# Kernel tuning notes

Hardware: AMD Instinct MI355X
Metric: run time of the kernel (lower is better)

## Reference

```python
import jax, jax.numpy as jnp
import numpy as np

N, E = 10000, 320000
C = 64          # channel multiplicity of 0e and 1o node features
A = 4           # node_attrs (species one-hot) dim
NB = 8          # radial basis size (edge_embedding dim)
H = 8           # invariant_neurons
AVG_NEIGH = 32.0
LOG2 = 0.6931471805599453

def ssp(x):
    # ShiftedSoftPlus
    return jax.nn.softplus(x) - LOG2


def setup_inputs() -> dict:
    key = jax.random.key(0)
    ks = jax.random.split(key, 13)
    d = dict(
        node_features=jax.random.normal(ks[0], (N, 4 * C), jnp.float32),   # [N, C + 3C]
        node_attrs=jax.random.normal(ks[1], (N, A), jnp.float32),
        edge_attrs=jax.random.normal(ks[2], (E, 4), jnp.float32),          # sh l=0,1
        edge_embedding=jax.random.uniform(ks[3], (E, NB), jnp.float32),
        edge_index=jax.random.randint(ks[4], (2, E), 0, N),
        # e3nn Linear (internal weights) per-l blocks
        W_lin1_0=jax.random.normal(ks[5], (C, C), jnp.float32),
        W_lin1_1=jax.random.normal(ks[6], (C, C), jnp.float32),
        # radial FullyConnectedNet: NB -> H -> 4C (tp.weight_numel)
        W_fc1=jax.random.normal(ks[7], (NB, H), jnp.float32),
        W_fc2=jax.random.normal(ks[8], (H, 4 * C), jnp.float32),
        # linear_2: irreps_mid.simplify() = 2Cx0e+2Cx1o -> Cx0e+Cx1o
        W_lin2_0=jax.random.normal(ks[9], (2 * C, C), jnp.float32),
        W_lin2_1=jax.random.normal(ks[10], (2 * C, C), jnp.float32),
        # self-connection FullyConnectedTensorProduct weights (node_attrs are scalars)
        W_sc0=jax.random.normal(ks[11], (C, A, C), jnp.float32),
        W_sc1=jax.random.normal(ks[12], (C, A, C), jnp.float32),
    )
    return d


def _forward(node_features, node_attrs, edge_attrs, edge_embedding, edge_index,
             W_lin1_0, W_lin1_1, W_fc1, W_fc2, W_lin2_0, W_lin2_1, W_sc0, W_sc1):
    n = node_features.shape[0]
    e = edge_attrs.shape[0]
    x0 = node_features[:, :C]                      # [N, C]   scalars (0e)
    x1 = node_features[:, C:].reshape(n, C, 3)     # [N, C, 3] vectors (1o)

    # self-connection: FullyConnectedTensorProduct(feat, node_attrs(0e)) -> feat
    sc_norm = 1.0 / np.sqrt(C * A)
    sc0 = jnp.einsum('nu,na,uav->nv', x0, node_attrs, W_sc0) * sc_norm
    sc1 = jnp.einsum('num,na,uav->nvm', x1, node_attrs, W_sc1) * sc_norm

    # linear_1 (per-irrep mixing, e3nn normalization 1/sqrt(fan_in))
    y0 = (x0 @ W_lin1_0) / np.sqrt(C)
    y1 = jnp.einsum('num,uv->nvm', x1, W_lin1_1) / np.sqrt(C)

    # radial MLP -> per-edge TP weights [E, 4C] (instruction order p1..p4)
    h = ssp((edge_embedding @ W_fc1) / np.sqrt(NB))
    w = (h @ W_fc2) / np.sqrt(H)
    wp1, wp2, wp3, wp4 = jnp.split(w, 4, axis=1)   # each [E, C]

    src = edge_index[1]
    dst = edge_index[0]
    xs0 = y0[src]                                  # [E, C]
    xs1 = y1[src]                                  # [E, C, 3]
    sh0 = edge_attrs[:, :1]                        # [E, 1]
    sh1 = edge_attrs[:, 1:4]                       # [E, 3]

    # uvu tensor product paths (component normalization)
    mid_s0 = wp1 * xs0 * sh0                                            # 0e x 0e -> 0e
    mid_s1 = wp4 * jnp.einsum('eum,em->eu', xs1, sh1) / np.sqrt(3.0)    # 1o x 1o -> 0e
    mid_v0 = (wp2 * xs0)[:, :, None] * sh1[:, None, :]                  # 0e x 1o -> 1o
    mid_v1 = wp3[:, :, None] * xs1 * sh0[:, :, None]                    # 1o x 0e -> 1o

    edge_feat = jnp.concatenate(
        [mid_s0, mid_s1, mid_v0.reshape(e, 3 * C), mid_v1.reshape(e, 3 * C)], axis=1
    )                                                                    # [E, 8C]

    # scatter-sum to destination nodes, then divide by sqrt(avg_num_neighbors)
    agg = jnp.zeros((n, 8 * C), edge_feat.dtype).at[dst].add(edge_feat)
    agg = agg / np.sqrt(AVG_NEIGH)

    s = agg[:, :2 * C]                              # [N, 2C] scalars
    v = agg[:, 2 * C:].reshape(n, 2 * C, 3)         # [N, 2C, 3] vectors

    # linear_2 on simplified mid irreps
    o0 = (s @ W_lin2_0) / np.sqrt(2 * C) + sc0
    o1 = jnp.einsum('num,uv->nvm', v, W_lin2_1) / np.sqrt(2 * C) + sc1

    return jnp.concatenate([o0, o1.reshape(n, 3 * C)], axis=1)          # [N, 4C]


def reference(node_features, node_attrs, edge_attrs, edge_embedding, edge_index,
              W_lin1_0, W_lin1_1, W_fc1, W_fc2, W_lin2_0, W_lin2_1, W_sc0, W_sc1):
    return _forward(node_features, node_attrs, edge_attrs, edge_embedding, edge_index,
                    W_lin1_0, W_lin1_1, W_fc1, W_fc2, W_lin2_0, W_lin2_1, W_sc0, W_sc1)
```

## Files before the change

### kernel.cpp

```cpp
#include <hip/hip_runtime.h>


__device__ __forceinline__ unsigned short f2b(float f) {
  unsigned u = __float_as_uint(f);
  return (unsigned short)((u + 0x7FFFu + ((u >> 16) & 1u)) >> 16);
}
__device__ __forceinline__ unsigned packb(float a, float b) {
  return (unsigned)f2b(a) | ((unsigned)f2b(b) << 16);
}
__device__ __forceinline__ float blo(unsigned p) { return __uint_as_float(p << 16); }
__device__ __forceinline__ float bhi(unsigned p) { return __uint_as_float(p & 0xFFFF0000u); }
__device__ __forceinline__ float b2f(unsigned short h) {
  return __uint_as_float((unsigned)h << 16);
}

__global__ __launch_bounds__(256) void k_pack(
    const float* __restrict__ W10, const float* __restrict__ W11,
    const float* __restrict__ Ws0, const float* __restrict__ Ws1,
    const float* __restrict__ W20, const float* __restrict__ W21,
    unsigned* __restrict__ wpk1, unsigned* __restrict__ wpks,
    unsigned* __restrict__ wpk2a, unsigned* __restrict__ wpk2b) {
  int i = blockIdx.x * 256 + threadIdx.x;
  if (i < 4096) wpk1[i] = packb(W10[i], W11[i]);
  else if (i < 4096 + 16384) {
    int j = i - 4096;
    wpks[j] = packb(Ws0[j], Ws1[j]);
  } else if (i < 4096 + 16384 + 4096) {
    int j = i - (4096 + 16384);
    wpk2a[j] = packb(W20[j], W20[4096 + j]);
  } else if (i < 4096 + 16384 + 8192) {
    int j = i - (4096 + 16384 + 4096);
    wpk2b[j] = packb(W21[j], W21[4096 + j]);
  }
}

__global__ __launch_bounds__(256) void k_hist(const int* __restrict__ ei,
                                              int* __restrict__ cnt, int nedges) {
  int e = blockIdx.x * 256 + threadIdx.x;
  if (e < nedges) atomicAdd(&cnt[ei[e]], 1);
}

__global__ __launch_bounds__(1024) void k_scan(const int* __restrict__ cnt,
                                               int* __restrict__ offs,
                                               int* __restrict__ cur,
                                               int nnodes, int nedges) {
  __shared__ int s_wtot[16], s_wpre[16];
  const int tid = threadIdx.x;
  const int lane = tid & 63;
  const int w = tid >> 6;
  int vals[16];
  int tot = 0;
  const int start = tid * 16;
#pragma unroll
  for (int k = 0; k < 16; ++k) {
    int i = start + k;
    int c = (i < nnodes) ? cnt[i] : 0;
    vals[k] = c;
    tot += c;
  }
  int incl = tot;
#pragma unroll
  for (int off = 1; off < 64; off <<= 1) {
    int v = __shfl_up(incl, off, 64);
    if (lane >= off) incl += v;
  }
  if (lane == 63) s_wtot[w] = incl;
  __syncthreads();
  if (tid == 0) {
    int run = 0;
#pragma unroll
    for (int i = 0; i < 16; ++i) { s_wpre[i] = run; run += s_wtot[i]; }
  }
  __syncthreads();
  int run = s_wpre[w] + (incl - tot);
#pragma unroll
  for (int k = 0; k < 16; ++k) {
    int i = start + k;
    if (i < nnodes) {
      offs[i] = run;
      cur[i] = run;
      run += vals[k];
    }
  }
  if (tid == 0) offs[nnodes] = nedges;
}

__global__ __launch_bounds__(256) void k_build(
    const int* __restrict__ ei, const float* __restrict__ ee,
    const float* __restrict__ ea, const float* __restrict__ Wf1,
    int* __restrict__ cur, int* __restrict__ srcs,
    uint4* __restrict__ erec, int nedges) {
  __shared__ float s_w[64];
  const int tid = threadIdx.x;
  if (tid < 64) s_w[tid] = Wf1[tid];
  __syncthreads();
  int e = blockIdx.x * 256 + tid;
  if (e >= nedges) return;
  const int d = ei[e];
  const int s = ei[nedges + e];
  const int p = atomicAdd(&cur[d], 1);
  srcs[p] = s;
  const float4 a = *(const float4*)(ee + (size_t)e * 8);
  const float4 b = *(const float4*)(ee + (size_t)e * 8 + 4);
  float r[8];
  const float is8 = 0.35355339059327379f;
#pragma unroll
  for (int j = 0; j < 8; ++j) {
    float dd = a.x * s_w[0 * 8 + j] + a.y * s_w[1 * 8 + j] + a.z * s_w[2 * 8 + j] +
               a.w * s_w[3 * 8 + j] + b.x * s_w[4 * 8 + j] + b.y * s_w[5 * 8 + j] +
               b.z * s_w[6 * 8 + j] + b.w * s_w[7 * 8 + j];
    dd *= is8;
    float sp = fmaxf(dd, 0.f) + log1pf(__expf(-fabsf(dd)));
    r[j] = (sp - 0.69314718055994531f) * is8;
  }
  const float4 sh = *(const float4*)(ea + (size_t)e * 4);
  erec[(size_t)p * 2] = make_uint4(packb(r[0], r[1]), packb(r[2], r[3]),
                                   packb(r[4], r[5]), packb(r[6], r[7]));
  erec[(size_t)p * 2 + 1] =
      make_uint4(__float_as_uint(sh.x), __float_as_uint(sh.y),
                 __float_as_uint(sh.z), __float_as_uint(sh.w));
}

__global__ __launch_bounds__(256) void k_node_pre(
    const float* __restrict__ nf, const float* __restrict__ na,
    const unsigned* __restrict__ wpk1, const unsigned* __restrict__ wpks,
    unsigned short* __restrict__ yqb, float* __restrict__ out, int nnodes) {
  __shared__ unsigned s_w1[4096];
  __shared__ unsigned s_ws[16384];
  __shared__ float s_nf[16][256];
  __shared__ float s_na[16][4];
  const int tid = threadIdx.x;
  const int lane = tid & 63;
  const int wv = tid >> 6;

  for (int i = tid; i < 4096; i += 256) s_w1[i] = wpk1[i];
  for (int i = tid; i < 16384; i += 256) s_ws[i] = wpks[i];

  const int ngroups = (nnodes + 15) / 16;
  for (int g = blockIdx.x; g < ngroups; g += gridDim.x) {
    const int base = g * 16;
    __syncthreads();
    for (int i = tid; i < 16 * 256; i += 256) {
      int r = i >> 8, c = i & 255;
      int n = base + r;
      s_nf[r][c] = (n < nnodes) ? nf[(size_t)n * 256 + c] : 0.f;
    }
    if (tid < 64) {
      int r = tid >> 2, c = tid & 3;
      int n = base + r;
      s_na[r][c] = (n < nnodes) ? na[(size_t)n * 4 + c] : 0.f;
    }
    __syncthreads();

    const int r0 = wv * 4;
    const int v = lane;
    float y0a[4] = {0.f, 0.f, 0.f, 0.f};
    float y1a[4][3] = {};
    float sc0a[4] = {0.f, 0.f, 0.f, 0.f};
    float sc1a[4][3] = {};

#pragma unroll 4
    for (int u = 0; u < 64; ++u) {
      float x0r[4], x1r[4][3];
#pragma unroll
      for (int r = 0; r < 4; ++r) {
        x0r[r] = s_nf[r0 + r][u];
#pragma unroll
        for (int m = 0; m < 3; ++m) x1r[r][m] = s_nf[r0 + r][64 + u * 3 + m];
      }
      const unsigned q1 = s_w1[u * 64 + v];
      const float w0 = blo(q1);
      const float w1 = bhi(q1);
#pragma unroll
      for (int r = 0; r < 4; ++r) {
        y0a[r] = fmaf(x0r[r], w0, y0a[r]);
#pragma unroll
        for (int m = 0; m < 3; ++m) y1a[r][m] = fmaf(x1r[r][m], w1, y1a[r][m]);
      }
#pragma unroll
      for (int a = 0; a < 4; ++a) {
        const unsigned qs = s_ws[(u * 4 + a) * 64 + v];
        const float ws0 = blo(qs);
        const float ws1 = bhi(qs);
#pragma unroll
        for (int r = 0; r < 4; ++r) {
          const float nav = s_na[r0 + r][a];
          sc0a[r] = fmaf(x0r[r] * nav, ws0, sc0a[r]);
          const float t = nav * ws1;
#pragma unroll
          for (int m = 0; m < 3; ++m)
            sc1a[r][m] = fmaf(x1r[r][m], t, sc1a[r][m]);
        }
      }
    }

#pragma unroll
    for (int r = 0; r < 4; ++r) {
      const int n = base + r0 + r;
      if (n < nnodes) {
        ushort4 yv;
        yv.x = f2b(y0a[r] * 0.125f);
        yv.y = f2b(y1a[r][0] * 0.125f);
        yv.z = f2b(y1a[r][1] * 0.125f);
        yv.w = f2b(y1a[r][2] * 0.125f);
        *(ushort4*)(yqb + ((size_t)n * 64 + v) * 4) = yv;
        out[(size_t)n * 256 + v] = sc0a[r] * 0.0625f;
#pragma unroll
        for (int m = 0; m < 3; ++m)
          out[(size_t)n * 256 + 64 + v * 3 + m] = sc1a[r][m] * 0.0625f;
      }
    }
  }
}

__global__ __launch_bounds__(256, 4) void k_agg(
    const unsigned short* __restrict__ yqb, const uint4* __restrict__ erec,
    const int* __restrict__ srcs, const int* __restrict__ offs,
    const float* __restrict__ Wf2, unsigned short* __restrict__ aggb, int nnodes) {
  const int tid = threadIdx.x;
  const int u = tid & 63;
  const int wv = tid >> 6;
  const int n = blockIdx.x * 4 + wv;
  if (n >= nnodes) return;

  float wreg[32];
#pragma unroll
  for (int j = 0; j < 8; ++j)
#pragma unroll
    for (int q = 0; q < 4; ++q) wreg[j * 4 + q] = Wf2[j * 256 + q * 64 + u];

  float as0 = 0.f, as1 = 0.f;
  float av0[3] = {0.f, 0.f, 0.f};
  float av1[3] = {0.f, 0.f, 0.f};

  const int beg = offs[n], end = offs[n + 1];
#pragma unroll 4
  for (int i = beg; i < end; ++i) {
    const int src = srcs[i];
    const ushort4 yb = *(const ushort4*)(yqb + ((size_t)src * 64 + u) * 4);
    const uint4 hp = erec[(size_t)i * 2];
    const uint4 shu = erec[(size_t)i * 2 + 1];
    const float4 sh = make_float4(__uint_as_float(shu.x), __uint_as_float(shu.y),
                                  __uint_as_float(shu.z), __uint_as_float(shu.w));
    const float hv[8] = {blo(hp.x), bhi(hp.x), blo(hp.y), bhi(hp.y),
                         blo(hp.z), bhi(hp.z), blo(hp.w), bhi(hp.w)};
    float wp[4] = {0.f, 0.f, 0.f, 0.f};
#pragma unroll
    for (int j = 0; j < 8; ++j)
#pragma unroll
      for (int q = 0; q < 4; ++q) wp[q] = fmaf(hv[j], wreg[j * 4 + q], wp[q]);
    const float y0 = b2f(yb.x), y1 = b2f(yb.y), y2 = b2f(yb.z), y3 = b2f(yb.w);
    const float dot3 = y1 * sh.y + y2 * sh.z + y3 * sh.w;
    as0 = fmaf(wp[0] * y0, sh.x, as0);
    as1 = fmaf(wp[3], dot3, as1);
    const float t2 = wp[1] * y0;
    av0[0] = fmaf(t2, sh.y, av0[0]);
    av0[1] = fmaf(t2, sh.z, av0[1]);
    av0[2] = fmaf(t2, sh.w, av0[2]);
    const float t3 = wp[2] * sh.x;
    av1[0] = fmaf(t3, y1, av1[0]);
    av1[1] = fmaf(t3, y2, av1[1]);
    av1[2] = fmaf(t3, y3, av1[2]);
  }

  unsigned short* ap = aggb + (size_t)n * 512;
  ap[u] = f2b(as0);
  ap[64 + u] = f2b(as1 * 0.57735026918962576f);
#pragma unroll
  for (int m = 0; m < 3; ++m) {
    ap[128 + m * 64 + u] = f2b(av0[m]);
    ap[320 + m * 64 + u] = f2b(av1[m]);
  }
}

__global__ __launch_bounds__(256, 4) void k_lin2(
    const unsigned short* __restrict__ aggb, const unsigned* __restrict__ wpk2a,
    const unsigned* __restrict__ wpk2b, float* __restrict__ out, int nnodes) {
  __shared__ float s_x[4][4][512];
  const int tid = threadIdx.x;
  const int u = tid & 63;
  const int wv = tid >> 6;
  const int nb = blockIdx.x * 16 + wv * 4;

#pragma unroll
  for (int r = 0; r < 4; ++r) {
    const int n = nb + r;
    if (n < nnodes) {
      const uint4 aw = *(const uint4*)(aggb + (size_t)n * 512 + u * 8);
      float4* dst = (float4*)&s_x[wv][r][u * 8];
      dst[0] = make_float4(blo(aw.x), bhi(aw.x), blo(aw.y), bhi(aw.y));
      dst[1] = make_float4(blo(aw.z), bhi(aw.z), blo(aw.w), bhi(aw.w));
    }
  }

  float o0[4] = {0.f, 0.f, 0.f, 0.f};
  float o1[4][3] = {};

#pragma unroll 2
  for (int up = 0; up < 64; ++up) {
    const unsigned qa = wpk2a[up * 64 + u];
    const unsigned qb = wpk2b[up * 64 + u];
    const float w20a = blo(qa), w20b = bhi(qa);
    const float w21a = blo(qb), w21b = bhi(qb);
#pragma unroll
    for (int r = 0; r < 4; ++r) {
      o0[r] = fmaf(s_x[wv][r][up], w20a, o0[r]);
      o0[r] = fmaf(s_x[wv][r][64 + up], w20b, o0[r]);
#pragma unroll
      for (int m = 0; m < 3; ++m) {
        o1[r][m] = fmaf(s_x[wv][r][128 + m * 64 + up], w21a, o1[r][m]);
        o1[r][m] = fmaf(s_x[wv][r][320 + m * 64 + up], w21b, o1[r][m]);
      }
    }
  }

  const float scl = 1.f / 64.f;
#pragma unroll
  for (int r = 0; r < 4; ++r) {
    const int n = nb + r;
    if (n < nnodes) {
      out[(size_t)n * 256 + u] += o0[r] * scl;
#pragma unroll
      for (int m = 0; m < 3; ++m)
        out[(size_t)n * 256 + 64 + u * 3 + m] += o1[r][m] * scl;
    }
  }
}

extern "C" void kernel_launch(void* const* d_in, const int* in_sizes, int n_in,
                              void* d_out, int out_size, void* d_ws, size_t ws_size,
                              hipStream_t stream) {
  const float* nf = (const float*)d_in[0];
  const float* na = (const float*)d_in[1];
  const float* ea = (const float*)d_in[2];
  const float* ee = (const float*)d_in[3];
  const int* ei = (const int*)d_in[4];
  const float* W10 = (const float*)d_in[5];
  const float* W11 = (const float*)d_in[6];
  const float* Wf1 = (const float*)d_in[7];
  const float* Wf2 = (const float*)d_in[8];
  const float* W20 = (const float*)d_in[9];
  const float* W21 = (const float*)d_in[10];
  const float* Ws0 = (const float*)d_in[11];
  const float* Ws1 = (const float*)d_in[12];
  float* out = (float*)d_out;

  const int N = in_sizes[1] / 4;
  const int E = in_sizes[2] / 4;

  char* w = (char*)d_ws;
  auto carve = [&](size_t bytes) {
    char* p = w;
    w += (bytes + 255) & ~(size_t)255;
    return p;
  };
  unsigned short* yqb = (unsigned short*)carve((size_t)N * 256 * 2);
  uint4* erec = (uint4*)carve((size_t)E * 32);
  unsigned short* aggb = (unsigned short*)carve((size_t)N * 512 * 2);
  unsigned* wpk1 = (unsigned*)carve(4096 * 4);
  unsigned* wpks = (unsigned*)carve(16384 * 4);
  unsigned* wpk2a = (unsigned*)carve(4096 * 4);
  unsigned* wpk2b = (unsigned*)carve(4096 * 4);
  int* cnt = (int*)carve((size_t)N * sizeof(int));
  int* offs = (int*)carve((size_t)(N + 1) * sizeof(int));
  int* cur = (int*)carve((size_t)N * sizeof(int));
  int* srcs = (int*)carve((size_t)E * sizeof(int));

  hipMemsetAsync(cnt, 0, (size_t)N * sizeof(int), stream);
  k_pack<<<(4096 + 16384 + 8192 + 255) / 256, 256, 0, stream>>>(
      W10, W11, Ws0, Ws1, W20, W21, wpk1, wpks, wpk2a, wpk2b);
  const int egrid = (E + 255) / 256;
  k_hist<<<egrid, 256, 0, stream>>>(ei, cnt, E);
  k_scan<<<1, 1024, 0, stream>>>(cnt, offs, cur, N, E);
  k_build<<<egrid, 256, 0, stream>>>(ei, ee, ea, Wf1, cur, srcs, erec, E);
  const int ngroups = (N + 15) / 16;
  const int npgrid = (ngroups < 256) ? ngroups : 256;
  k_node_pre<<<npgrid, 256, 0, stream>>>(nf, na, wpk1, wpks, yqb, out, N);
  k_agg<<<(N + 3) / 4, 256, 0, stream>>>(yqb, erec, srcs, offs, Wf2, aggb, N);
  k_lin2<<<(N + 15) / 16, 256, 0, stream>>>(aggb, wpk2a, wpk2b, out, N);
}
```

Before: 311.4 us.

## Use bf16 MFMA for node pre-linear/self-connection and linear_2 kernels

Rewrites k_node_pre and k_lin2 to use 16x16x32 bf16 MFMA instructions instead of scalar FMA loops. Weights are pre-packed into MFMA fragment layout, with the self-connection weights concatenated alongside lin1 so a single GEMM produces both outputs. The node_attrs contraction is then applied to the accumulator in registers. Node features are converted to bf16 and stored in swizzled shared memory, and the persistent grid becomes one block per 64 nodes. This adds bf16 rounding of the node features and a large LDS footprint (about 120KB) in node_pre, which may limit occupancy.

```diff
diff --git a/kernel.cpp b/kernel.cpp
--- a/kernel.cpp
+++ b/kernel.cpp
@@ -1,5 +1,8 @@
 #include <hip/hip_runtime.h>
 
+
+typedef __attribute__((ext_vector_type(8))) short bf16x8;
+typedef __attribute__((ext_vector_type(4))) float f32x4;
 
 __device__ __forceinline__ unsigned short f2b(float f) {
   unsigned u = __float_as_uint(f);
@@ -18,19 +21,26 @@
     const float* __restrict__ W10, const float* __restrict__ W11,
     const float* __restrict__ Ws0, const float* __restrict__ Ws1,
     const float* __restrict__ W20, const float* __restrict__ W21,
-    unsigned* __restrict__ wpk1, unsigned* __restrict__ wpks,
-    unsigned* __restrict__ wpk2a, unsigned* __restrict__ wpk2b) {
+    unsigned short* __restrict__ fb0, unsigned short* __restrict__ fb1,
+    unsigned short* __restrict__ fw20, unsigned short* __restrict__ fw21) {
   int i = blockIdx.x * 256 + threadIdx.x;
-  if (i < 4096) wpk1[i] = packb(W10[i], W11[i]);
-  else if (i < 4096 + 16384) {
-    int j = i - 4096;
-    wpks[j] = packb(Ws0[j], Ws1[j]);
-  } else if (i < 4096 + 16384 + 4096) {
-    int j = i - (4096 + 16384);
-    wpk2a[j] = packb(W20[j], W20[4096 + j]);
-  } else if (i < 4096 + 16384 + 8192) {
-    int j = i - (4096 + 16384 + 4096);
-    wpk2b[j] = packb(W21[j], W21[4096 + j]);
+  if (i < 20480) {
+    int j = i & 7, lane = (i >> 3) & 63;
+    int f = i >> 9;
+    int ct = f % 20, kt = f / 20;
+    int k = kt * 32 + ((lane >> 4) << 3) + j;
+    int c = ct * 16 + (lane & 15);
+    fb0[i] = f2b(c < 256 ? Ws0[k * 256 + c] : W10[k * 64 + (c - 256)]);
+    fb1[i] = f2b(c < 256 ? Ws1[k * 256 + c] : W11[k * 64 + (c - 256)]);
+  } else if (i < 20480 + 8192) {
+    int t = i - 20480;
+    int j = t & 7, lane = (t >> 3) & 63;
+    int f = t >> 9;
+    int ct = f & 3, kt = f >> 2;
+    int k = kt * 32 + ((lane >> 4) << 3) + j;
+    int c = ct * 16 + (lane & 15);
+    fw20[t] = f2b(W20[k * 64 + c]);
+    fw21[t] = f2b(W21[k * 64 + c]);
   }
 }
 
@@ -123,92 +133,114 @@
 
 __global__ __launch_bounds__(256) void k_node_pre(
     const float* __restrict__ nf, const float* __restrict__ na,
-    const unsigned* __restrict__ wpk1, const unsigned* __restrict__ wpks,
+    const unsigned short* __restrict__ fb0, const unsigned short* __restrict__ fb1,
     unsigned short* __restrict__ yqb, float* __restrict__ out, int nnodes) {
-  __shared__ unsigned s_w1[4096];
-  __shared__ unsigned s_ws[16384];
-  __shared__ float s_nf[16][256];
-  __shared__ float s_na[16][4];
+  __shared__ __align__(16) unsigned short s_b0[20480];
+  __shared__ __align__(16) unsigned short s_b1[20480];
+  __shared__ __align__(16) unsigned short s_p[4][64][64];
+  __shared__ __align__(16) float4 s_na4[64];
+  __shared__ __align__(16) unsigned short s_y[4][16][64][4];
   const int tid = threadIdx.x;
-  const int lane = tid & 63;
-  const int wv = tid >> 6;
-
-  for (int i = tid; i < 4096; i += 256) s_w1[i] = wpk1[i];
-  for (int i = tid; i < 16384; i += 256) s_ws[i] = wpks[i];
-
-  const int ngroups = (nnodes + 15) / 16;
-  for (int g = blockIdx.x; g < ngroups; g += gridDim.x) {
-    const int base = g * 16;
-    __syncthreads();
-    for (int i = tid; i < 16 * 256; i += 256) {
-      int r = i >> 8, c = i & 255;
-      int n = base + r;
-      s_nf[r][c] = (n < nnodes) ? nf[(size_t)n * 256 + c] : 0.f;
-    }
-    if (tid < 64) {
-      int r = tid >> 2, c = tid & 3;
-      int n = base + r;
-      s_na[r][c] = (n < nnodes) ? na[(size_t)n * 4 + c] : 0.f;
-    }
-    __syncthreads();
-
-    const int r0 = wv * 4;
-    const int v = lane;
-    float y0a[4] = {0.f, 0.f, 0.f, 0.f};
-    float y1a[4][3] = {};
-    float sc0a[4] = {0.f, 0.f, 0.f, 0.f};
-    float sc1a[4][3] = {};
-
-#pragma unroll 4
-    for (int u = 0; u < 64; ++u) {
-      float x0r[4], x1r[4][3];
+  const int l = tid & 63;
+  const int w = tid >> 6;
+  const int base = blockIdx.x * 64;
+
+  for (int i = tid; i < 2560; i += 256) {
+    ((uint4*)s_b0)[i] = ((const uint4*)fb0)[i];
+    ((uint4*)s_b1)[i] = ((const uint4*)fb1)[i];
+  }
+  for (int c = tid; c < 2048; c += 256) {
+    int p = c >> 9, ln = (c >> 3) & 63, c8 = c & 7;
+    int n = base + ln;
+    unsigned short v[8];
+    if (n < nnodes) {
+      const float* row = nf + (size_t)n * 256;
+      if (p == 0) {
+#pragma unroll
+        for (int j = 0; j < 8; ++j) v[j] = f2b(row[c8 * 8 + j]);
+      } else {
+        int m = p - 1;
+#pragma unroll
+        for (int j = 0; j < 8; ++j) v[j] = f2b(row[64 + (c8 * 8 + j) * 3 + m]);
+      }
+    } else {
+#pragma unroll
+      for (int j = 0; j < 8; ++j) v[j] = 0;
+    }
+    *(uint4*)&s_p[p][ln][(c8 ^ (ln & 7)) * 8] = *(uint4*)v;
+  }
+  {
+    int ln = tid >> 2, a = tid & 3;
+    int n = base + ln;
+    ((float*)&s_na4[ln])[a] = (n < nnodes) ? na[(size_t)n * 4 + a] : 0.f;
+  }
+  __syncthreads();
+
+  const int ln0 = w * 16;
+  bf16x8 af[4][2];
+  {
+    const int ln = ln0 + (l & 15);
+#pragma unroll
+    for (int p = 0; p < 4; ++p)
+#pragma unroll
+      for (int kt = 0; kt < 2; ++kt) {
+        int c8 = kt * 4 + (l >> 4);
+        af[p][kt] = *(const bf16x8*)&s_p[p][ln][(c8 ^ (ln & 7)) * 8];
+      }
+  }
+  float narf[4][4];
+#pragma unroll
+  for (int r = 0; r < 4; ++r) {
+    float4 nv = s_na4[ln0 + (l >> 4) * 4 + r];
+    narf[r][0] = nv.x; narf[r][1] = nv.y; narf[r][2] = nv.z; narf[r][3] = nv.w;
+  }
+
+#pragma unroll
+  for (int q = 0; q < 4; ++q) {
+    const unsigned short* sb = (q == 0) ? s_b0 : s_b1;
+    float scr[4][4] = {};
+#pragma unroll
+    for (int ct = 0; ct < 20; ++ct) {
+      f32x4 acc = {0.f, 0.f, 0.f, 0.f};
+#pragma unroll
+      for (int kt = 0; kt < 2; ++kt) {
+        bf16x8 bf = *(const bf16x8*)&sb[((kt * 20 + ct) * 64 + l) * 8];
+        acc = __builtin_amdgcn_mfma_f32_16x16x32_bf16(af[q][kt], bf, acc, 0, 0, 0);
+      }
+      if (ct < 16) {
+        const int a = ct >> 2, vt = ct & 3;
+#pragma unroll
+        for (int r = 0; r < 4; ++r)
+          scr[vt][r] = fmaf(narf[r][a], acc[r], scr[vt][r]);
+      } else {
+        const int vt = ct - 16;
+#pragma unroll
+        for (int r = 0; r < 4; ++r)
+          s_y[w][(l >> 4) * 4 + r][vt * 16 + (l & 15)][q] = f2b(acc[r] * 0.125f);
+      }
+    }
+#pragma unroll
+    for (int vt = 0; vt < 4; ++vt)
 #pragma unroll
       for (int r = 0; r < 4; ++r) {
-        x0r[r] = s_nf[r0 + r][u];
-#pragma unroll
-        for (int m = 0; m < 3; ++m) x1r[r][m] = s_nf[r0 + r][64 + u * 3 + m];
-      }
-      const unsigned q1 = s_w1[u * 64 + v];
-      const float w0 = blo(q1);
-      const float w1 = bhi(q1);
-#pragma unroll
-      for (int r = 0; r < 4; ++r) {
-        y0a[r] = fmaf(x0r[r], w0, y0a[r]);
-#pragma unroll
-        for (int m = 0; m < 3; ++m) y1a[r][m] = fmaf(x1r[r][m], w1, y1a[r][m]);
-      }
-#pragma unroll
-      for (int a = 0; a < 4; ++a) {
-        const unsigned qs = s_ws[(u * 4 + a) * 64 + v];
-        const float ws0 = blo(qs);
-        const float ws1 = bhi(qs);
-#pragma unroll
-        for (int r = 0; r < 4; ++r) {
-          const float nav = s_na[r0 + r][a];
-          sc0a[r] = fmaf(x0r[r] * nav, ws0, sc0a[r]);
-          const float t = nav * ws1;
-#pragma unroll
-          for (int m = 0; m < 3; ++m)
-            sc1a[r][m] = fmaf(x1r[r][m], t, sc1a[r][m]);
+        const int n = base + ln0 + (l >> 4) * 4 + r;
+        if (n < nnodes) {
+          const int v = vt * 16 + (l & 15);
+          const float val = scr[vt][r] * 0.0625f;
+          if (q == 0) out[(size_t)n * 256 + v] = val;
+          else out[(size_t)n * 256 + 64 + v * 3 + (q - 1)] = val;
         }
       }
-    }
-
-#pragma unroll
-    for (int r = 0; r < 4; ++r) {
-      const int n = base + r0 + r;
-      if (n < nnodes) {
-        ushort4 yv;
-        yv.x = f2b(y0a[r] * 0.125f);
-        yv.y = f2b(y1a[r][0] * 0.125f);
-        yv.z = f2b(y1a[r][1] * 0.125f);
-        yv.w = f2b(y1a[r][2] * 0.125f);
-        *(ushort4*)(yqb + ((size_t)n * 64 + v) * 4) = yv;
-        out[(size_t)n * 256 + v] = sc0a[r] * 0.0625f;
-#pragma unroll
-        for (int m = 0; m < 3; ++m)
-          out[(size_t)n * 256 + 64 + v * 3 + m] = sc1a[r][m] * 0.0625f;
-      }
+  }
+
+#pragma unroll
+  for (int i = 0; i < 16; ++i) {
+    int idx = i * 64 + l;
+    int node = idx >> 6, v = idx & 63;
+    int n = base + ln0 + node;
+    if (n < nnodes) {
+      ushort4 t = *(ushort4*)&s_y[w][node][v][0];
+      *(ushort4*)(yqb + ((size_t)n * 64 + v) * 4) = t;
     }
   }
 }
@@ -273,56 +305,56 @@
   }
 }
 
-__global__ __launch_bounds__(256, 4) void k_lin2(
-    const unsigned short* __restrict__ aggb, const unsigned* __restrict__ wpk2a,
-    const unsigned* __restrict__ wpk2b, float* __restrict__ out, int nnodes) {
-  __shared__ float s_x[4][4][512];
+__global__ __launch_bounds__(256) void k_lin2(
+    const unsigned short* __restrict__ aggb, const unsigned short* __restrict__ fw20,
+    const unsigned short* __restrict__ fw21, float* __restrict__ out, int nnodes) {
+  __shared__ __align__(16) unsigned short s_w[2][8192];
   const int tid = threadIdx.x;
-  const int u = tid & 63;
-  const int wv = tid >> 6;
-  const int nb = blockIdx.x * 16 + wv * 4;
-
-#pragma unroll
-  for (int r = 0; r < 4; ++r) {
-    const int n = nb + r;
-    if (n < nnodes) {
-      const uint4 aw = *(const uint4*)(aggb + (size_t)n * 512 + u * 8);
-      float4* dst = (float4*)&s_x[wv][r][u * 8];
-      dst[0] = make_float4(blo(aw.x), bhi(aw.x), blo(aw.y), bhi(aw.y));
-      dst[1] = make_float4(blo(aw.z), bhi(aw.z), blo(aw.w), bhi(aw.w));
-    }
-  }
-
-  float o0[4] = {0.f, 0.f, 0.f, 0.f};
-  float o1[4][3] = {};
-
-#pragma unroll 2
-  for (int up = 0; up < 64; ++up) {
-    const unsigned qa = wpk2a[up * 64 + u];
-    const unsigned qb = wpk2b[up * 64 + u];
-    const float w20a = blo(qa), w20b = bhi(qa);
-    const float w21a = blo(qb), w21b = bhi(qb);
-#pragma unroll
-    for (int r = 0; r < 4; ++r) {
-      o0[r] = fmaf(s_x[wv][r][up], w20a, o0[r]);
-      o0[r] = fmaf(s_x[wv][r][64 + up], w20b, o0[r]);
-#pragma unroll
-      for (int m = 0; m < 3; ++m) {
-        o1[r][m] = fmaf(s_x[wv][r][128 + m * 64 + up], w21a, o1[r][m]);
-        o1[r][m] = fmaf(s_x[wv][r][320 + m * 64 + up], w21b, o1[r][m]);
-      }
-    }
-  }
-
-  const float scl = 1.f / 64.f;
-#pragma unroll
-  for (int r = 0; r < 4; ++r) {
-    const int n = nb + r;
-    if (n < nnodes) {
-      out[(size_t)n * 256 + u] += o0[r] * scl;
-#pragma unroll
-      for (int m = 0; m < 3; ++m)
-        out[(size_t)n * 256 + 64 + u * 3 + m] += o1[r][m] * scl;
+  const int l = tid & 63;
+  const int w = tid >> 6;
+  const int base = blockIdx.x * 64;
+
+  for (int i = tid; i < 1024; i += 256) {
+    ((uint4*)s_w[0])[i] = ((const uint4*)fw20)[i];
+    ((uint4*)s_w[1])[i] = ((const uint4*)fw21)[i];
+  }
+  __syncthreads();
+
+  const int ln0 = w * 16;
+  int nrow = base + ln0 + (l & 15);
+  if (nrow >= nnodes) nrow = nnodes - 1;
+  const unsigned short* arow = aggb + (size_t)nrow * 512;
+
+#pragma unroll
+  for (int q = 0; q < 4; ++q) {
+    bf16x8 af[4];
+#pragma unroll
+    for (int kt = 0; kt < 4; ++kt) {
+      int k = kt * 32 + ((l >> 4) << 3);
+      int off = (q == 0) ? k
+                         : (k < 64 ? 128 + (q - 1) * 64 + k
+                                   : 320 + (q - 1) * 64 + (k - 64));
+      af[kt] = *(const bf16x8*)(arow + off);
+    }
+    const unsigned short* sw = (q == 0) ? s_w[0] : s_w[1];
+#pragma unroll
+    for (int ct = 0; ct < 4; ++ct) {
+      f32x4 acc = {0.f, 0.f, 0.f, 0.f};
+#pragma unroll
+      for (int kt = 0; kt < 4; ++kt) {
+        bf16x8 bf = *(const bf16x8*)&sw[((kt * 4 + ct) * 64 + l) * 8];
+        acc = __builtin_amdgcn_mfma_f32_16x16x32_bf16(af[kt], bf, acc, 0, 0, 0);
+      }
+#pragma unroll
+      for (int r = 0; r < 4; ++r) {
+        const int n = base + ln0 + (l >> 4) * 4 + r;
+        if (n < nnodes) {
+          const int v = ct * 16 + (l & 15);
+          const size_t o =
+              (size_t)n * 256 + ((q == 0) ? v : 64 + v * 3 + (q - 1));
+          out[o] += acc[r] * 0.015625f;
+        }
+      }
     }
   }
 }
@@ -357,25 +389,24 @@
   unsigned short* yqb = (unsigned short*)carve((size_t)N * 256 * 2);
   uint4* erec = (uint4*)carve((size_t)E * 32);
   unsigned short* aggb = (unsigned short*)carve((size_t)N * 512 * 2);
-  unsigned* wpk1 = (unsigned*)carve(4096 * 4);
-  unsigned* wpks = (unsigned*)carve(16384 * 4);
-  unsigned* wpk2a = (unsigned*)carve(4096 * 4);
-  unsigned* wpk2b = (unsigned*)carve(4096 * 4);
+  unsigned short* fb0 = (unsigned short*)carve(20480 * 2);
+  unsigned short* fb1 = (unsigned short*)carve(20480 * 2);
+  unsigned short* fw20 = (unsigned short*)carve(8192 * 2);
+  unsigned short* fw21 = (unsigned short*)carve(8192 * 2);
   int* cnt = (int*)carve((size_t)N * sizeof(int));
   int* offs = (int*)carve((size_t)(N + 1) * sizeof(int));
   int* cur = (int*)carve((size_t)N * sizeof(int));
   int* srcs = (int*)carve((size_t)E * sizeof(int));
 
   hipMemsetAsync(cnt, 0, (size_t)N * sizeof(int), stream);
-  k_pack<<<(4096 + 16384 + 8192 + 255) / 256, 256, 0, stream>>>(
-      W10, W11, Ws0, Ws1, W20, W21, wpk1, wpks, wpk2a, wpk2b);
+  k_pack<<<(20480 + 8192 + 255) / 256, 256, 0, stream>>>(
+      W10, W11, Ws0, Ws1, W20, W21, fb0, fb1, fw20, fw21);
   const int egrid = (E + 255) / 256;
   k_hist<<<egrid, 256, 0, stream>>>(ei, cnt, E);
   k_scan<<<1, 1024, 0, stream>>>(cnt, offs, cur, N, E);
   k_build<<<egrid, 256, 0, stream>>>(ei, ee, ea, Wf1, cur, srcs, erec, E);
-  const int ngroups = (N + 15) / 16;
-  const int npgrid = (ngroups < 256) ? ngroups : 256;
-  k_node_pre<<<npgrid, 256, 0, stream>>>(nf, na, wpk1, wpks, yqb, out, N);
+  const int ngrid = (N + 63) / 64;
+  k_node_pre<<<ngrid, 256, 0, stream>>>(nf, na, fb0, fb1, yqb, out, N);
   k_agg<<<(N + 3) / 4, 256, 0, stream>>>(yqb, erec, srcs, offs, Wf2, aggb, N);
-  k_lin2<<<(N + 15) / 16, 256, 0, stream>>>(aggb, wpk2a, wpk2b, out, N);
-}
+  k_lin2<<<ngrid, 256, 0, stream>>>(aggb, fw20, fw21, out, N);
+}
```

Measured after the change: 249.3 us. 1.25x faster.
